# Kernel optimization log

Hardware: AMD Instinct MI355X
Metric: run time of the kernel (lower is better)

Reference implementation:

```python
import jax, jax.numpy as jnp
from jax import lax
import numpy as np

B, C_IN, H, W = 4, 3, 128, 128
K, D = 8192, 16  # num_embeddings, embedding_size (= encoder out channels)


def _conv(x, w, b):
    # x: (B,C,H,W), w: (O,I,3,3) OIHW, VALID padding, stride 1
    y = lax.conv_general_dilated(x, w, (1, 1), 'VALID',
                                 dimension_numbers=('NCHW', 'OIHW', 'NCHW'))
    return y + b[None, :, None, None]


def _conv_t(x, w, b):
    # transpose conv, stride 1, k=3: correlate with flipped/transposed kernel, pad 2
    # w: (I,O,3,3) -> flip spatial, swap to OIHW
    wk = jnp.flip(w, (2, 3)).transpose(1, 0, 2, 3)
    y = lax.conv_general_dilated(x, wk, (1, 1), [(2, 2), (2, 2)],
                                 dimension_numbers=('NCHW', 'OIHW', 'NCHW'))
    return y + b[None, :, None, None]


def setup_inputs() -> dict:
    key = jax.random.key(0)
    ks = jax.random.split(key, 14)
    g = lambda k, shp, fan: jax.random.normal(k, shp, jnp.float32) / np.float32(np.sqrt(fan))
    return {
        'x':   jax.random.normal(ks[0], (B, C_IN, H, W), jnp.float32),
        'ew1': g(ks[1], (4, C_IN, 3, 3), C_IN * 9), 'eb1': jnp.zeros((4,), jnp.float32),
        'ew2': g(ks[2], (8, 4, 3, 3), 4 * 9),       'eb2': jnp.zeros((8,), jnp.float32),
        'ew3': g(ks[3], (16, 8, 3, 3), 8 * 9),      'eb3': jnp.zeros((16,), jnp.float32),
        'dw1': g(ks[4], (16, 8, 3, 3), 16 * 9),     'db1': jnp.zeros((8,), jnp.float32),
        'dw2': g(ks[5], (8, 4, 3, 3), 8 * 9),       'db2': jnp.zeros((4,), jnp.float32),
        'dw3': g(ks[6], (4, C_IN, 3, 3), 4 * 9),    'db3': jnp.zeros((C_IN,), jnp.float32),
        'codebook': jax.random.normal(ks[7], (K, D), jnp.float32) * 0.02,
    }


def reference(x, ew1, eb1, ew2, eb2, ew3, eb3, dw1, db1, dw2, db2, dw3, db3, codebook):
    # encode
    z = jax.nn.selu(_conv(x, ew1, eb1))
    z = jax.nn.selu(_conv(z, ew2, eb2))
    z = _conv(z, ew3, eb3)                      # (B, D, h, w)
    b, d, h, w = z.shape
    zf = z.transpose(0, 2, 3, 1).reshape(-1, d)  # (N, D) flattened latents
    # ||z - e||^2 = ||z||^2 - 2 z.e + ||e||^2, argmin over codebook rows
    d2 = ((zf * zf).sum(1, keepdims=True)
          - 2.0 * (zf @ codebook.T)
          + (codebook * codebook).sum(1)[None, :])  # (N, K)
    idx = jnp.argmin(d2, axis=1)                 # (N,) int32
    zq = codebook[idx].reshape(b, h, w, d).transpose(0, 3, 1, 2)  # gather + reshape
    # decode
    y = jax.nn.selu(_conv_t(zq, dw1, db1))
    y = jax.nn.selu(_conv_t(y, dw2, db2))
    y = _conv_t(y, dw3, db3)                     # (B, C_IN, H, W)
    return (y, idx)
```

## Files before the change

kernel.cpp:

```cpp
#include <hip/hip_runtime.h>
#include <math.h>

#define BATCH 4
#define DLAT 16
#define KCB 8192
#define HLAT 122
#define PIX (HLAT*HLAT)
#define NLAT (BATCH*PIX)
#define NT32 (KCB/32)
#define ROWSB 32
#define NVQBLK 1861
#define NWAVE 4
#define TW (NT32/NWAVE)
#define CAPW 1024
#define NCONVBLK 3721

typedef _Float16 half8 __attribute__((ext_vector_type(8)));
typedef float f32x16 __attribute__((ext_vector_type(16)));

__device__ __forceinline__ float selu_np(float x) {
    const float scale = 1.0507009873554805f, alpha = 1.6732632423543772f;
    if (x > 0.f) return __fmul_rn(scale, x);
    return __fmul_rn(scale, __fmul_rn(alpha, expm1f(x)));
}

template<int CI, int CO, int HIN, int WIN, bool DOSELU>
__global__ void conv3x3_np(const float* __restrict__ in, const float* __restrict__ w,
                           const float* __restrict__ bias, float* __restrict__ out) {
    constexpr int HO = HIN - 2, WO = WIN - 2;
    int tid = blockIdx.x * blockDim.x + threadIdx.x;
    constexpr int total = BATCH * CO * HO * WO;
    if (tid >= total) return;
    int j = tid % WO; int t = tid / WO;
    int i = t % HO;   t /= HO;
    int o = t % CO;   int b = t / CO;
    float acc = 0.f;
    for (int c = 0; c < CI; ++c) {
        const float* ip = in + ((b * CI + c) * HIN + i) * WIN + j;
        const float* wp = w + ((o * CI + c) * 3) * 3;
        #pragma unroll
        for (int p = 0; p < 3; ++p)
            #pragma unroll
            for (int q = 0; q < 3; ++q)
                acc = __fmaf_rn(ip[p * WIN + q], wp[p * 3 + q], acc);
    }
    acc = __fadd_rn(acc, bias[o]);
    out[tid] = DOSELU ? selu_np(acc) : acc;
}

__global__ void conv3_last_np(const float* __restrict__ in, const float* __restrict__ w,
                              const float* __restrict__ bias, float* __restrict__ zf,
                              _Float16* __restrict__ zh, float* __restrict__ blockmax) {
    constexpr int CI = 8, HIN = 124, WIN = 124, WO = 122;
    __shared__ float sred[4];
    int tid = blockIdx.x * 256 + threadIdx.x;
    int o  = tid & 15;
    int pp = tid >> 4;
    int b = pp / PIX, pix = pp % PIX;
    int i = pix / WO, j = pix % WO;
    float acc = 0.f;
    for (int c = 0; c < CI; ++c) {
        const float* ip = in + ((b * CI + c) * HIN + i) * WIN + j;
        const float* wp = w + ((o * CI + c) * 3) * 3;
        #pragma unroll
        for (int p = 0; p < 3; ++p)
            #pragma unroll
            for (int q = 0; q < 3; ++q)
                acc = __fmaf_rn(ip[p * WIN + q], wp[p * 3 + q], acc);
    }
    acc = __fadd_rn(acc, bias[o]);
    zf[tid] = acc;
    zh[tid] = (_Float16)acc;
    float m = fabsf(acc);
    #pragma unroll
    for (int off = 32; off; off >>= 1) m = fmaxf(m, __shfl_xor(m, off));
    if ((threadIdx.x & 63) == 0) sred[threadIdx.x >> 6] = m;
    __syncthreads();
    if (threadIdx.x == 0)
        blockmax[blockIdx.x] = fmaxf(fmaxf(sred[0], sred[1]), fmaxf(sred[2], sred[3]));
}

__global__ void reduce_zmax(const float* __restrict__ bm, unsigned* __restrict__ scal) {
    __shared__ float sred[4];
    float m = 0.f;
    for (int i = threadIdx.x; i < NCONVBLK; i += 256) m = fmaxf(m, bm[i]);
    #pragma unroll
    for (int off = 32; off; off >>= 1) m = fmaxf(m, __shfl_xor(m, off));
    if ((threadIdx.x & 63) == 0) sred[threadIdx.x >> 6] = m;
    __syncthreads();
    if (threadIdx.x == 0)
        scal[0] = __float_as_uint(fmaxf(fmaxf(sred[0], sred[1]), fmaxf(sred[2], sred[3])));
    if (threadIdx.x == 1) scal[1] = 0u;
}

__device__ __forceinline__ float pairwise16_sq(const float* v) {
    float a[16];
    #pragma unroll
    for (int d = 0; d < 16; ++d) a[d] = __fmul_rn(v[d], v[d]);
    float r0 = __fadd_rn(a[0], a[8]),  r1 = __fadd_rn(a[1], a[9]);
    float r2 = __fadd_rn(a[2], a[10]), r3 = __fadd_rn(a[3], a[11]);
    float r4 = __fadd_rn(a[4], a[12]), r5 = __fadd_rn(a[5], a[13]);
    float r6 = __fadd_rn(a[6], a[14]), r7 = __fadd_rn(a[7], a[15]);
    return __fadd_rn(__fadd_rn(__fadd_rn(r0, r1), __fadd_rn(r2, r3)),
                     __fadd_rn(__fadd_rn(r4, r5), __fadd_rn(r6, r7)));
}

__device__ __forceinline__ void load16(const float* __restrict__ p, float* v) {
    const float4* r = (const float4*)p;
    float4 v0 = r[0], v1 = r[1], v2 = r[2], v3 = r[3];
    v[0]=v0.x; v[1]=v0.y; v[2]=v0.z; v[3]=v0.w;
    v[4]=v1.x; v[5]=v1.y; v[6]=v1.z; v[7]=v1.w;
    v[8]=v2.x; v[9]=v2.y; v[10]=v2.z; v[11]=v2.w;
    v[12]=v3.x; v[13]=v3.y; v[14]=v3.z; v[15]=v3.w;
}

__device__ __forceinline__ float np_d2(const float* zr, float A, const float* e16, float cnk) {
    float g = 0.f;
    #pragma unroll
    for (int d = 0; d < 16; ++d) g = __fmaf_rn(zr[d], e16[d], g);
    return __fadd_rn(__fmaf_rn(-2.f, g, A), cnk);
}

__global__ void cbprep(const float* __restrict__ cb, float* __restrict__ cn,
                       float* __restrict__ cnT,
                       _Float16* __restrict__ cbB, unsigned* __restrict__ scal) {
    int k = blockIdx.x * 256 + threadIdx.x;
    float v[16];
    load16(cb + (size_t)k * DLAT, v);
    float C = pairwise16_sq(v);
    cn[k] = C;
    int tile = k >> 5, col = k & 31;
    cnT[col * NT32 + tile] = __fmul_rn(-0.5f, C);
    float m = C;
    #pragma unroll
    for (int off = 32; off; off >>= 1) m = fmaxf(m, __shfl_xor(m, off));
    if ((threadIdx.x & 63) == 0) atomicMax(&scal[1], __float_as_uint(m));
    #pragma unroll
    for (int d = 0; d < 16; ++d) {
        int ln = (d >> 3) * 32 + col;
        cbB[(size_t)tile * 512 + ln * 8 + (d & 7)] = (_Float16)v[d];
    }
}

#define DROW(reg, lanehi) (((reg) & 3) + 8 * ((reg) >> 2) + 4 * (lanehi))

__global__ __launch_bounds__(256, 4) void vq_mfma(
        const _Float16* __restrict__ zh, const float* __restrict__ zf,
        const _Float16* __restrict__ cbB, const float* __restrict__ cn,
        const float* __restrict__ cnT,
        const float* __restrict__ cb, const unsigned* __restrict__ scal,
        float* __restrict__ idx_out, float* __restrict__ zq) {
    __shared__ unsigned list[CAPW];
    __shared__ float resd[CAPW];
    __shared__ float smax[NWAVE][ROWSB];
    __shared__ unsigned lcnt;
    const int tid = threadIdx.x;
    const int w = tid >> 6, lane = tid & 63;
    const int lanehi = lane >> 5;
    const int col = lane & 31;
    const int R0 = blockIdx.x * ROWSB;
    if (tid == 0) lcnt = 0;

    int ar = R0 + col;
    if (ar >= NLAT) ar = NLAT - 1;
    half8 a = *(const half8*)(zh + (size_t)ar * DLAT + lanehi * 8);

    float zmaxf = __uint_as_float(scal[0]);
    float en    = sqrtf(__uint_as_float(scal[1]));
    float errG  = 4.f * zmaxf * en * 9.765625e-4f * 1.03f
                + 6.104e-5f * (16.f * zmaxf + 4.f * en);
    float slack = (16.f * zmaxf * zmaxf + 8.f * zmaxf * en + en * en) * 1.2e-7f;
    float DELTA = 4.f * errG + 2.f * slack + 1e-6f;

    const int t0 = w * TW, t1 = t0 + TW;
    const float* cnTl = cnT + (size_t)col * NT32;

    float mm[16];
    #pragma unroll
    for (int r = 0; r < 16; ++r) mm[r] = -INFINITY;

    for (int t = t0; t < t1; t += 4) {
        float4 cn4 = *(const float4*)(cnTl + t);
        #pragma unroll
        for (int u = 0; u < 4; ++u) {
            half8 b = *(const half8*)(cbB + (size_t)(t + u) * 512 + lane * 8);
            float cnv = ((const float*)&cn4)[u];
            f32x16 cvec;
            #pragma unroll
            for (int j = 0; j < 16; ++j) cvec[j] = cnv;
            f32x16 D = __builtin_amdgcn_mfma_f32_32x32x16_f16(a, b, cvec, 0, 0, 0);
            #pragma unroll
            for (int r = 0; r < 16; ++r) mm[r] = fmaxf(mm[r], D[r]);
        }
    }
    #pragma unroll
    for (int r = 0; r < 16; ++r) {
        float v = mm[r];
        v = fmaxf(v, __shfl_xor(v, 1));
        v = fmaxf(v, __shfl_xor(v, 2));
        v = fmaxf(v, __shfl_xor(v, 4));
        v = fmaxf(v, __shfl_xor(v, 8));
        v = fmaxf(v, __shfl_xor(v, 16));
        mm[r] = v;
    }
    if (col == 0) {
        #pragma unroll
        for (int r = 0; r < 16; ++r)
            smax[w][DROW(r, lanehi)] = mm[r];
    }
    __syncthreads();
    #pragma unroll
    for (int r = 0; r < 16; ++r) {
        int row = DROW(r, lanehi);
        float v = -INFINITY;
        #pragma unroll
        for (int ww = 0; ww < NWAVE; ++ww) v = fmaxf(v, smax[ww][row]);
        mm[r] = v - 0.5f * DELTA;
    }

    for (int t = t0; t < t1; t += 4) {
        float4 cn4 = *(const float4*)(cnTl + t);
        #pragma unroll
        for (int u = 0; u < 4; ++u) {
            half8 b = *(const half8*)(cbB + (size_t)(t + u) * 512 + lane * 8);
            float cnv = ((const float*)&cn4)[u];
            f32x16 cvec;
            #pragma unroll
            for (int j = 0; j < 16; ++j) cvec[j] = cnv;
            f32x16 D = __builtin_amdgcn_mfma_f32_32x32x16_f16(a, b, cvec, 0, 0, 0);
            bool anyp = false;
            #pragma unroll
            for (int r = 0; r < 16; ++r)
                anyp |= (D[r] >= mm[r]);
            if (__ballot(anyp)) {
                #pragma unroll
                for (int r = 0; r < 16; ++r) {
                    bool pred = (D[r] >= mm[r]);
                    unsigned long long bal = __ballot(pred);
                    if (bal) {
                        unsigned nb = (unsigned)__popcll(bal);
                        unsigned base = 0;
                        if (lane == 0) base = atomicAdd(&lcnt, nb);
                        base = __shfl(base, 0);
                        unsigned pos = base + (unsigned)__popcll(bal & ((1ull << lane) - 1ull));
                        if (pred && pos < CAPW) {
                            unsigned rs = (unsigned)DROW(r, lanehi);
                            list[pos] = (rs << 13) | (unsigned)((t + u) * 32 + col);
                        }
                    }
                }
            }
        }
    }
    __syncthreads();
    unsigned cnt = lcnt;

    if (cnt <= CAPW) {
        for (unsigned i = tid; i < cnt; i += 256) {
            unsigned e = list[i];
            int n = R0 + (int)(e >> 13);
            if (n >= NLAT) n = NLAT - 1;
            int k = (int)(e & 8191);
            float zr[16], e16[16];
            load16(zf + (size_t)n * DLAT, zr);
            float A = pairwise16_sq(zr);
            load16(cb + (size_t)k * DLAT, e16);
            resd[i] = np_d2(zr, A, e16, cn[k]);
        }
    }
    __syncthreads();

    if (tid < ROWSB) {
        int r = R0 + tid;
        if (r < NLAT) {
            float bd = INFINITY; int bk = 0x7fffffff;
            if (cnt <= CAPW) {
                for (unsigned i = 0; i < cnt; ++i) {
                    unsigned e = list[i];
                    if ((int)(e >> 13) == tid) {
                        float d2 = resd[i]; int k = (int)(e & 8191);
                        if (d2 < bd || (d2 == bd && k < bk)) { bd = d2; bk = k; }
                    }
                }
            } else {
                float zr[16];
                load16(zf + (size_t)r * DLAT, zr);
                float A = pairwise16_sq(zr);
                for (int k = 0; k < KCB; ++k) {
                    float e16[16];
                    load16(cb + (size_t)k * DLAT, e16);
                    float d2 = np_d2(zr, A, e16, cn[k]);
                    if (d2 < bd) { bd = d2; bk = k; }
                }
            }
            idx_out[r] = (float)bk;
            int b = r / PIX, pix = r % PIX;
            const float* e = cb + (size_t)bk * DLAT;
            #pragma unroll
            for (int d = 0; d < DLAT; ++d) zq[((size_t)(b * DLAT + d)) * PIX + pix] = e[d];
        }
    }
}

template<int CI, int CO, int HIN, int WIN, bool DOSELU>
__global__ void convt3x3(const float* __restrict__ in, const float* __restrict__ w,
                         const float* __restrict__ bias, float* __restrict__ out) {
    constexpr int HO = HIN + 2, WO = WIN + 2;
    int tid = blockIdx.x * blockDim.x + threadIdx.x;
    constexpr int total = BATCH * CO * HO * WO;
    if (tid >= total) return;
    int j = tid % WO; int t = tid / WO;
    int i = t % HO;   t /= HO;
    int o = t % CO;   int b = t / CO;
    float acc = bias[o];
    for (int c = 0; c < CI; ++c) {
        const float* ip = in + ((b * CI + c) * HIN) * WIN;
        const float* wp = w + ((c * CO + o) * 3) * 3;
        #pragma unroll
        for (int p = 0; p < 3; ++p) {
            int ii = i + p - 2;
            if (ii < 0 || ii >= HIN) continue;
            #pragma unroll
            for (int q = 0; q < 3; ++q) {
                int jj = j + q - 2;
                if (jj < 0 || jj >= WIN) continue;
                acc += ip[ii * WIN + jj] * wp[(2 - p) * 3 + (2 - q)];
            }
        }
    }
    const float scale = 1.0507009873554805f, alpha = 1.6732632423543772f;
    out[tid] = DOSELU ? (acc > 0.f ? scale * acc : scale * alpha * (expf(acc) - 1.f)) : acc;
}

extern "C" void kernel_launch(void* const* d_in, const int* in_sizes, int n_in,
                              void* d_out, int out_size, void* d_ws, size_t ws_size,
                              hipStream_t stream) {
    const float* x   = (const float*)d_in[0];
    const float* ew1 = (const float*)d_in[1];  const float* eb1 = (const float*)d_in[2];
    const float* ew2 = (const float*)d_in[3];  const float* eb2 = (const float*)d_in[4];
    const float* ew3 = (const float*)d_in[5];  const float* eb3 = (const float*)d_in[6];
    const float* dw1 = (const float*)d_in[7];  const float* db1 = (const float*)d_in[8];
    const float* dw2 = (const float*)d_in[9];  const float* db2 = (const float*)d_in[10];
    const float* dw3 = (const float*)d_in[11]; const float* db3 = (const float*)d_in[12];
    const float* cb  = (const float*)d_in[13];

    float* out_y   = (float*)d_out;
    float* out_idx = (float*)d_out + 196608;

    float*     ws   = (float*)d_ws;
    float*     zf   = ws;
    float*     e1   = ws + 952576;
    float*     e2   = ws + 1206592;
    float*     fZq  = ws + 952576;
    float*     fB   = ws + 1905152;
    float*     fA   = ws + 2397184;
    _Float16*  zh   = (_Float16*)(ws + 2651200);
    _Float16*  cbB  = (_Float16*)(ws + 3127488);
    float*     cn   = ws + 3193024;
    float*     cnT  = ws + 3201216;
    unsigned*  scal = (unsigned*)(ws + 3209408);
    float*     bmax = ws + 3209410;

    const int TPB = 256;

    conv3x3_np<3, 4, 128, 128, true ><<<993,  TPB, 0, stream>>>(x,  ew1, eb1, e1);
    conv3x3_np<4, 8, 126, 126, true ><<<1922, TPB, 0, stream>>>(e1, ew2, eb2, e2);
    conv3_last_np<<<NCONVBLK, TPB, 0, stream>>>(e2, ew3, eb3, zf, zh, bmax);
    reduce_zmax<<<1, TPB, 0, stream>>>(bmax, scal);

    cbprep<<<32, TPB, 0, stream>>>(cb, cn, cnT, cbB, scal);
    vq_mfma<<<NVQBLK, TPB, 0, stream>>>(zh, zf, cbB, cn, cnT, cb, scal, out_idx, fZq);

    convt3x3<16, 8, 122, 122, true ><<<1922, TPB, 0, stream>>>(fZq, dw1, db1, fB);
    convt3x3<8, 4, 124, 124, true ><<<993,  TPB, 0, stream>>>(fB,  dw2, db2, fA);
    convt3x3<4, 3, 126, 126, false><<<768,  TPB, 0, stream>>>(fA,  dw3, db3, out_y);
}
```

Baseline: 222.8 us.

## Replace two-pass VQ max scan with single-pass running-min candidate filter

The VQ kernel no longer runs a full first pass over the codebook to find each row's best score. It seeds a per-lane running minimum from a few tiles, then does one pass that updates that minimum and records candidates within DELTA of it. If the candidate list overflows, a fallback rescans the codebook with the block-wide threshold. Separately, the transpose-conv gets a branch-free interior path that skips bounds checks. The risks are more candidates early in the scan, a larger shared-memory list (CAPW doubled), and extra VALU work per MFMA.

```diff
diff --git a/kernel.cpp b/kernel.cpp
--- a/kernel.cpp
+++ b/kernel.cpp
@@ -12,7 +12,8 @@
 #define NVQBLK 1861
 #define NWAVE 4
 #define TW (NT32/NWAVE)
-#define CAPW 1024
+#define SEED 8
+#define CAPW 2048
 #define NCONVBLK 3721
 
 typedef _Float16 half8 __attribute__((ext_vector_type(8)));
@@ -130,7 +131,7 @@
     float C = pairwise16_sq(v);
     cn[k] = C;
     int tile = k >> 5, col = k & 31;
-    cnT[col * NT32 + tile] = __fmul_rn(-0.5f, C);
+    cnT[col * NT32 + tile] = C;
     float m = C;
     #pragma unroll
     for (int off = 32; off; off >>= 1) m = fmaxf(m, __shfl_xor(m, off));
@@ -152,13 +153,14 @@
         float* __restrict__ idx_out, float* __restrict__ zq) {
     __shared__ unsigned list[CAPW];
     __shared__ float resd[CAPW];
-    __shared__ float smax[NWAVE][ROWSB];
+    __shared__ float smin[NWAVE][ROWSB];
     __shared__ unsigned lcnt;
     const int tid = threadIdx.x;
     const int w = tid >> 6, lane = tid & 63;
     const int lanehi = lane >> 5;
     const int col = lane & 31;
     const int R0 = blockIdx.x * ROWSB;
+    const f32x16 zero16 = {0.f,0.f,0.f,0.f,0.f,0.f,0.f,0.f,0.f,0.f,0.f,0.f,0.f,0.f,0.f,0.f};
     if (tid == 0) lcnt = 0;
 
     int ar = R0 + col;
@@ -175,47 +177,31 @@
     const int t0 = w * TW, t1 = t0 + TW;
     const float* cnTl = cnT + (size_t)col * NT32;
 
-    float mm[16];
-    #pragma unroll
-    for (int r = 0; r < 16; ++r) mm[r] = -INFINITY;
-
-    for (int t = t0; t < t1; t += 4) {
+    float known[16];
+    #pragma unroll
+    for (int r = 0; r < 16; ++r) known[r] = INFINITY;
+
+    for (int t = t0; t < t0 + SEED; t += 4) {
         float4 cn4 = *(const float4*)(cnTl + t);
         #pragma unroll
         for (int u = 0; u < 4; ++u) {
             half8 b = *(const half8*)(cbB + (size_t)(t + u) * 512 + lane * 8);
             float cnv = ((const float*)&cn4)[u];
-            f32x16 cvec;
-            #pragma unroll
-            for (int j = 0; j < 16; ++j) cvec[j] = cnv;
-            f32x16 D = __builtin_amdgcn_mfma_f32_32x32x16_f16(a, b, cvec, 0, 0, 0);
-            #pragma unroll
-            for (int r = 0; r < 16; ++r) mm[r] = fmaxf(mm[r], D[r]);
+            f32x16 D = __builtin_amdgcn_mfma_f32_32x32x16_f16(a, b, zero16, 0, 0, 0);
+            #pragma unroll
+            for (int r = 0; r < 16; ++r)
+                known[r] = fminf(known[r], __fmaf_rn(-2.f, D[r], cnv));
         }
     }
     #pragma unroll
     for (int r = 0; r < 16; ++r) {
-        float v = mm[r];
-        v = fmaxf(v, __shfl_xor(v, 1));
-        v = fmaxf(v, __shfl_xor(v, 2));
-        v = fmaxf(v, __shfl_xor(v, 4));
-        v = fmaxf(v, __shfl_xor(v, 8));
-        v = fmaxf(v, __shfl_xor(v, 16));
-        mm[r] = v;
-    }
-    if (col == 0) {
-        #pragma unroll
-        for (int r = 0; r < 16; ++r)
-            smax[w][DROW(r, lanehi)] = mm[r];
-    }
-    __syncthreads();
-    #pragma unroll
-    for (int r = 0; r < 16; ++r) {
-        int row = DROW(r, lanehi);
-        float v = -INFINITY;
-        #pragma unroll
-        for (int ww = 0; ww < NWAVE; ++ww) v = fmaxf(v, smax[ww][row]);
-        mm[r] = v - 0.5f * DELTA;
+        float v = known[r];
+        v = fminf(v, __shfl_xor(v, 1));
+        v = fminf(v, __shfl_xor(v, 2));
+        v = fminf(v, __shfl_xor(v, 4));
+        v = fminf(v, __shfl_xor(v, 8));
+        v = fminf(v, __shfl_xor(v, 16));
+        known[r] = v;
     }
 
     for (int t = t0; t < t1; t += 4) {
@@ -224,18 +210,19 @@
         for (int u = 0; u < 4; ++u) {
             half8 b = *(const half8*)(cbB + (size_t)(t + u) * 512 + lane * 8);
             float cnv = ((const float*)&cn4)[u];
-            f32x16 cvec;
-            #pragma unroll
-            for (int j = 0; j < 16; ++j) cvec[j] = cnv;
-            f32x16 D = __builtin_amdgcn_mfma_f32_32x32x16_f16(a, b, cvec, 0, 0, 0);
+            f32x16 D = __builtin_amdgcn_mfma_f32_32x32x16_f16(a, b, zero16, 0, 0, 0);
+            float sv[16];
             bool anyp = false;
             #pragma unroll
-            for (int r = 0; r < 16; ++r)
-                anyp |= (D[r] >= mm[r]);
+            for (int r = 0; r < 16; ++r) {
+                sv[r] = __fmaf_rn(-2.f, D[r], cnv);
+                known[r] = fminf(known[r], sv[r]);
+                anyp |= (sv[r] <= known[r] + DELTA);
+            }
             if (__ballot(anyp)) {
                 #pragma unroll
                 for (int r = 0; r < 16; ++r) {
-                    bool pred = (D[r] >= mm[r]);
+                    bool pred = (sv[r] <= known[r] + DELTA);
                     unsigned long long bal = __ballot(pred);
                     if (bal) {
                         unsigned nb = (unsigned)__popcll(bal);
@@ -255,6 +242,71 @@
     __syncthreads();
     unsigned cnt = lcnt;
 
+    if (cnt > CAPW) {
+        float thr[16];
+        #pragma unroll
+        for (int r = 0; r < 16; ++r) {
+            float v = known[r];
+            v = fminf(v, __shfl_xor(v, 1));
+            v = fminf(v, __shfl_xor(v, 2));
+            v = fminf(v, __shfl_xor(v, 4));
+            v = fminf(v, __shfl_xor(v, 8));
+            v = fminf(v, __shfl_xor(v, 16));
+            thr[r] = v;
+        }
+        if (col == 0) {
+            #pragma unroll
+            for (int r = 0; r < 16; ++r) smin[w][DROW(r, lanehi)] = thr[r];
+        }
+        __syncthreads();
+        #pragma unroll
+        for (int r = 0; r < 16; ++r) {
+            int row = DROW(r, lanehi);
+            float v = INFINITY;
+            #pragma unroll
+            for (int ww = 0; ww < NWAVE; ++ww) v = fminf(v, smin[ww][row]);
+            thr[r] = v + DELTA;
+        }
+        if (tid == 0) lcnt = 0;
+        __syncthreads();
+        for (int t = t0; t < t1; t += 4) {
+            float4 cn4 = *(const float4*)(cnTl + t);
+            #pragma unroll
+            for (int u = 0; u < 4; ++u) {
+                half8 b = *(const half8*)(cbB + (size_t)(t + u) * 512 + lane * 8);
+                float cnv = ((const float*)&cn4)[u];
+                f32x16 D = __builtin_amdgcn_mfma_f32_32x32x16_f16(a, b, zero16, 0, 0, 0);
+                bool anyp = false;
+                float sv[16];
+                #pragma unroll
+                for (int r = 0; r < 16; ++r) {
+                    sv[r] = __fmaf_rn(-2.f, D[r], cnv);
+                    anyp |= (sv[r] <= thr[r]);
+                }
+                if (__ballot(anyp)) {
+                    #pragma unroll
+                    for (int r = 0; r < 16; ++r) {
+                        bool pred = (sv[r] <= thr[r]);
+                        unsigned long long bal = __ballot(pred);
+                        if (bal) {
+                            unsigned nb = (unsigned)__popcll(bal);
+                            unsigned base = 0;
+                            if (lane == 0) base = atomicAdd(&lcnt, nb);
+                            base = __shfl(base, 0);
+                            unsigned pos = base + (unsigned)__popcll(bal & ((1ull << lane) - 1ull));
+                            if (pred && pos < CAPW) {
+                                unsigned rs = (unsigned)DROW(r, lanehi);
+                                list[pos] = (rs << 13) | (unsigned)((t + u) * 32 + col);
+                            }
+                        }
+                    }
+                }
+            }
+        }
+        __syncthreads();
+        cnt = lcnt;
+    }
+
     if (cnt <= CAPW) {
         for (unsigned i = tid; i < cnt; i += 256) {
             unsigned e = list[i];
@@ -313,18 +365,31 @@
     int i = t % HO;   t /= HO;
     int o = t % CO;   int b = t / CO;
     float acc = bias[o];
-    for (int c = 0; c < CI; ++c) {
-        const float* ip = in + ((b * CI + c) * HIN) * WIN;
-        const float* wp = w + ((c * CO + o) * 3) * 3;
-        #pragma unroll
-        for (int p = 0; p < 3; ++p) {
-            int ii = i + p - 2;
-            if (ii < 0 || ii >= HIN) continue;
-            #pragma unroll
-            for (int q = 0; q < 3; ++q) {
-                int jj = j + q - 2;
-                if (jj < 0 || jj >= WIN) continue;
-                acc += ip[ii * WIN + jj] * wp[(2 - p) * 3 + (2 - q)];
+    if (i >= 2 && i < HIN && j >= 2 && j < WIN) {
+        const float* ip0 = in + (((size_t)b * CI) * HIN + (i - 2)) * WIN + (j - 2);
+        for (int c = 0; c < CI; ++c) {
+            const float* ip = ip0 + (size_t)c * HIN * WIN;
+            const float* wp = w + ((c * CO + o) * 3) * 3;
+            #pragma unroll
+            for (int p = 0; p < 3; ++p)
+                #pragma unroll
+                for (int q = 0; q < 3; ++q)
+                    acc += ip[p * WIN + q] * wp[(2 - p) * 3 + (2 - q)];
+        }
+    } else {
+        for (int c = 0; c < CI; ++c) {
+            const float* ip = in + ((b * CI + c) * HIN) * WIN;
+            const float* wp = w + ((c * CO + o) * 3) * 3;
+            #pragma unroll
+            for (int p = 0; p < 3; ++p) {
+                int ii = i + p - 2;
+                if (ii < 0 || ii >= HIN) continue;
+                #pragma unroll
+                for (int q = 0; q < 3; ++q) {
+                    int jj = j + q - 2;
+                    if (jj < 0 || jj >= WIN) continue;
+                    acc += ip[ii * WIN + jj] * wp[(2 - p) * 3 + (2 - q)];
+                }
             }
         }
     }
```

New measurement: 723.0 us. 224% more time.
